# Optimization experiments

Measured on AMD Instinct MI355X. Metric: run time of the kernel, lower is better.

## Reference

```python
import jax, jax.numpy as jnp
import numpy as np

N_NODES = 100000
N_EDGES = 3200000
IN_DIM = 62
OUT_DIM = 16
EDGE_DIM = 2


def setup_inputs() -> dict:
    key = jax.random.key(0)
    ks = jax.random.split(key, 8)
    h = jax.random.normal(ks[0], (N_NODES, IN_DIM), dtype=jnp.float32)
    e = jax.random.normal(ks[1], (N_EDGES, EDGE_DIM), dtype=jnp.float32)
    src = jax.random.randint(ks[2], (N_EDGES,), 0, N_NODES, dtype=jnp.int32)
    dst = jax.random.randint(ks[3], (N_EDGES,), 0, N_NODES, dtype=jnp.int32)
    # xavier-normal-ish scaled weights
    W_fc = jax.random.normal(ks[4], (OUT_DIM, IN_DIM), dtype=jnp.float32) * 0.2
    W_attn = jax.random.normal(ks[5], (1, 2 * OUT_DIM + EDGE_DIM), dtype=jnp.float32) * 0.2
    W_edge = jax.random.normal(ks[6], (EDGE_DIM, EDGE_DIM), dtype=jnp.float32) * 0.5
    W_e2n = jax.random.normal(ks[7], (OUT_DIM, EDGE_DIM), dtype=jnp.float32) * 0.5
    return {"h": h, "e": e, "src": src, "dst": dst, "W_fc": W_fc,
            "W_attn": W_attn, "W_edge": W_edge, "W_e2n": W_e2n}


def _agat_forward(h, e, src, dst, W_fc, W_attn, W_edge, W_e2n):
    n = h.shape[0]
    d = W_fc.shape[0]
    z = h @ W_fc.T                      # [N, D]
    ex = e @ W_edge.T                   # [E, edge_dim]
    # attn_fc([z_src, z_dst, ex]) split into per-part projections
    Wa_src = W_attn[:, :d]              # [1, D]
    Wa_dst = W_attn[:, d:2 * d]         # [1, D]
    Wa_e = W_attn[:, 2 * d:]            # [1, edge_dim]
    a_src = (z @ Wa_src.T)[:, 0]        # [N] per-node, gathered per-edge
    a_dst = (z @ Wa_dst.T)[:, 0]        # [N]
    a = a_src[src] + a_dst[dst] + (ex @ Wa_e.T)[:, 0]   # [E]
    e_att = jax.nn.leaky_relu(a, negative_slope=0.01)    # [E]
    # segment softmax over incoming edges of each dst node
    m = jax.ops.segment_max(e_att, dst, num_segments=n)  # [N]
    w = jnp.exp(e_att - m[dst])                           # [E]
    denom = jax.ops.segment_sum(w, dst, num_segments=n)   # [N]
    attn = w / denom[dst]                                  # [E]
    # message = z_src + ez; aggregated as attn-weighted sum (matches
    # sum(attn*z) + sum(attn*ez) in reduce_func)
    ez = ex @ W_e2n.T                                      # [E, D]
    msg = attn[:, None] * (z[src] + ez)                    # [E, D]
    return jax.ops.segment_sum(msg, dst, num_segments=n)   # [N, D]


def reference(h, e, src, dst, W_fc, W_attn, W_edge, W_e2n):
    return _agat_forward(h, e, src, dst, W_fc, W_attn, W_edge, W_e2n)
```

## Files before the change

### kernel.cpp

```cpp
#include <hip/hip_runtime.h>
#include <hip/hip_fp16.h>
#include <hip/hip_cooperative_groups.h>

namespace cg = cooperative_groups;

#define N_NODES 100000
#define N_EDGES 3200000
#define IN_DIM  62
#define OUT_DIM 16

#define EBC    4096
#define EPT    4
#define NEB    ((N_EDGES + EBC - 1) / EBC)
#define NPB    ((N_NODES + 1023) / 1024)
#define NBUCK  ((N_NODES + 63) / 64)
#define CAPL   4096
#define CSTR   16
#define NCU    256

typedef int nat_i2 __attribute__((ext_vector_type(2)));

struct AppendSh {
    int  cnt[NBUCK];
    int  pfx[NBUCK];
    int  combo[NBUCK];
    int2 pay[EBC];
    unsigned short pbkt[EBC];
    int  wsum[16];
};
struct GatherSh {
    int2 rec[CAPL];
    unsigned short inv[CAPL];
    unsigned int exb[CAPL];
    int hist[64], pfx[64], cur[64];
    float adst_l[64];
};
union ShArena { AppendSh a; GatherSh g; };

__device__ __forceinline__ void do_proj(
    int u, int tid,
    const float* __restrict__ h, const float* __restrict__ W_fc,
    const float* __restrict__ W_attn,
    __half* __restrict__ zh, float* __restrict__ a_src_arr,
    float* __restrict__ a_dst_arr)
{
    int i = u * 1024 + tid;
    if (i >= N_NODES) return;

    float acc[OUT_DIM];
#pragma unroll
    for (int j = 0; j < OUT_DIM; ++j) acc[j] = 0.f;

    const float2* __restrict__ hr = (const float2*)(h + (size_t)i * IN_DIM);
#pragma unroll
    for (int kk = 0; kk < IN_DIM / 2; ++kk) {
        float2 hv = hr[kk];
#pragma unroll
        for (int j = 0; j < OUT_DIM; ++j) {
            acc[j] += hv.x * W_fc[j * IN_DIM + 2 * kk]
                    + hv.y * W_fc[j * IN_DIM + 2 * kk + 1];
        }
    }

    float asrc = 0.f, adst = 0.f;
#pragma unroll
    for (int j = 0; j < OUT_DIM; ++j) {
        asrc += acc[j] * W_attn[j];
        adst += acc[j] * W_attn[OUT_DIM + j];
    }

    union { __half hx[16]; uint4 q[2]; } uq;
#pragma unroll
    for (int j = 0; j < OUT_DIM; ++j) uq.hx[j] = __float2half(acc[j]);
    uint4* __restrict__ zrow = (uint4*)(zh + (size_t)i * OUT_DIM);
    zrow[0] = uq.q[0];
    zrow[1] = uq.q[1];

    a_src_arr[i] = asrc;
    a_dst_arr[i] = adst;
}

__device__ __forceinline__ void do_append(
    int be, int tid, AppendSh& S,
    const float* __restrict__ e, const int* __restrict__ src,
    const int* __restrict__ dst, int* __restrict__ cursor,
    nat_i2* __restrict__ records, int cap)
{
    __syncthreads();

    long ebase = (long)be * EBC;
    int chunk_n = (int)min((long)EBC, (long)N_EDGES - ebase);

    int dv[EPT], sv[EPT];
    float2 ev[EPT];
#pragma unroll
    for (int j = 0; j < EPT; ++j) {
        int p = tid + j * 1024;
        dv[j] = -1;
        if (p < chunk_n) {
            long eid = ebase + p;
            dv[j] = dst[eid];
            sv[j] = src[eid];
            ev[j] = ((const float2*)e)[eid];
        }
    }

    for (int t = tid; t < NBUCK; t += 1024) S.cnt[t] = 0;
    __syncthreads();

#pragma unroll
    for (int j = 0; j < EPT; ++j)
        if (dv[j] >= 0) atomicAdd(&S.cnt[dv[j] >> 6], 1);
    __syncthreads();

    int b0 = 2 * tid, b1 = b0 + 1;
    int c0 = (b0 < NBUCK) ? S.cnt[b0] : 0;
    int c1 = (b1 < NBUCK) ? S.cnt[b1] : 0;
    if (b0 < NBUCK) S.cnt[b0] = 0;
    if (b1 < NBUCK) S.cnt[b1] = 0;
    int gb0 = 0, gb1 = 0;
    if (c0) gb0 = atomicAdd(&cursor[b0 * CSTR], c0);
    if (c1) gb1 = atomicAdd(&cursor[b1 * CSTR], c1);

    int ts = c0 + c1;
    {
        int lane = tid & 63, wid = tid >> 6;
        int x = ts;
#pragma unroll
        for (int off = 1; off < 64; off <<= 1) {
            int y = __shfl_up(x, off, 64);
            if (lane >= off) x += y;
        }
        if (lane == 63) S.wsum[wid] = x;
        __syncthreads();
        if (wid == 0) {
            int v = (lane < 16) ? S.wsum[lane] : 0;
#pragma unroll
            for (int off = 1; off < 16; off <<= 1) {
                int y = __shfl_up(v, off, 64);
                if (lane >= off) v += y;
            }
            if (lane < 16) S.wsum[lane] = v;
        }
        __syncthreads();
        int texcl = x - ts + (wid ? S.wsum[wid - 1] : 0);
        if (b0 < NBUCK) { S.pfx[b0] = texcl;      S.combo[b0] = b0 * cap + gb0 - texcl; }
        if (b1 < NBUCK) { S.pfx[b1] = texcl + c0; S.combo[b1] = b1 * cap + gb1 - (texcl + c0); }
    }
    __syncthreads();

#pragma unroll
    for (int j = 0; j < EPT; ++j) {
        if (dv[j] >= 0) {
            int b = dv[j] >> 6;
            union { __half2 h2; int i; } uu;
            uu.h2.x = __float2half(ev[j].x);
            uu.h2.y = __float2half(ev[j].y);
            int r = atomicAdd(&S.cnt[b], 1);
            int q = S.pfx[b] + r;
            S.pay[q]  = make_int2(uu.i, sv[j] | ((dv[j] & 63) << 17));
            S.pbkt[q] = (unsigned short)b;
        }
    }
    __syncthreads();

    for (int p = tid; p < chunk_n; p += 1024) {
        int2 v  = S.pay[p];
        int  bb = S.pbkt[p];
        int pos = S.combo[bb] + p;
        if (pos < (bb + 1) * cap) {
            nat_i2 vv; vv.x = v.x; vv.y = v.y;
            __builtin_nontemporal_store(vv, records + pos);
        }
    }
}

__device__ __forceinline__ void do_gather(
    int b, int tid, GatherSh& S,
    const int* __restrict__ cursor, const nat_i2* __restrict__ records,
    const __half* __restrict__ zh, const float* __restrict__ a_src_arr,
    const float* __restrict__ a_dst_arr, const float* __restrict__ W_attn,
    const float* __restrict__ W_edge, const float* __restrict__ W_e2n,
    float* __restrict__ out, int cap)
{
    __syncthreads();

    long lo = (long)b * cap;
    int n   = cursor[b * CSTR];
    int nl  = n < cap ? n : cap;

    if (tid < 64) {
        S.hist[tid] = 0; S.cur[tid] = 0;
        int node = (b << 6) + tid;
        S.adst_l[tid] = (node < N_NODES) ? a_dst_arr[node] : 0.f;
    }
    __syncthreads();

    float we00 = W_edge[0], we01 = W_edge[1], we10 = W_edge[2], we11 = W_edge[3];
    float wa0  = W_attn[2 * OUT_DIM], wa1 = W_attn[2 * OUT_DIM + 1];

    int ld0 = -1, ld1 = -1, ld2 = -1, ld3 = -1;
#define EDGEW(J, LD)                                                        \
    {                                                                       \
        int k = tid + (J) * 1024;                                           \
        if (k < nl) {                                                       \
            nat_i2 r = __builtin_nontemporal_load(records + lo + k);        \
            int s  = r.y & 0x1FFFF;                                         \
            LD     = (r.y >> 17) & 63;                                      \
            union { int i; __half2 h2; } ue; ue.i = r.x;                    \
            float e0 = __low2float(ue.h2), e1 = __high2float(ue.h2);        \
            float ex0 = e0 * we00 + e1 * we01;                              \
            float ex1 = e0 * we10 + e1 * we11;                              \
            float a = a_src_arr[s] + S.adst_l[LD] + ex0 * wa0 + ex1 * wa1;  \
            float ea = (a > 0.f) ? a : 0.01f * a;                           \
            float w  = __expf(ea);                                          \
            S.rec[k] = make_int2(__float_as_int(w), r.y);                   \
            union { unsigned int i; __half2 h2; } up;                       \
            up.h2.x = __float2half(ex0);                                    \
            up.h2.y = __float2half(ex1);                                    \
            S.exb[k] = up.i;                                                \
            atomicAdd(&S.hist[LD], 1);                                      \
        }                                                                   \
    }
    EDGEW(0, ld0) EDGEW(1, ld1) EDGEW(2, ld2) EDGEW(3, ld3)
#undef EDGEW
    __syncthreads();

    if (tid < 64) S.pfx[tid] = S.hist[tid];
    __syncthreads();
    for (int off = 1; off < 64; off <<= 1) {
        int t = 0;
        if (tid < 64 && tid >= off) t = S.pfx[tid - off];
        __syncthreads();
        if (tid < 64) S.pfx[tid] += t;
        __syncthreads();
    }
    if (tid < 64) S.pfx[tid] -= S.hist[tid];
    __syncthreads();

#define INVW(J, LD)                                                         \
    if (LD >= 0) {                                                          \
        int k = tid + (J) * 1024;                                           \
        int r = atomicAdd(&S.cur[LD], 1);                                   \
        S.inv[S.pfx[LD] + r] = (unsigned short)k;                           \
    }
    INVW(0, ld0) INVW(1, ld1) INVW(2, ld2) INVW(3, ld3)
#undef INVW
    __syncthreads();

    int ld   = tid >> 4;
    int lane = tid & 15;
    int node = (b << 6) + ld;

    int m    = S.hist[ld];
    int base = S.pfx[ld];

    float acc0 = 0.f, acc1 = 0.f, accw0 = 0.f, accw1 = 0.f;
    float ax00 = 0.f, ax01 = 0.f, ax10 = 0.f, ax11 = 0.f;

    int i = 0;
    for (; i + 1 < m; i += 2) {
        int k0 = S.inv[base + i];
        int k1 = S.inv[base + i + 1];
        int2 r0 = S.rec[k0];
        int2 r1 = S.rec[k1];
        float w0 = __int_as_float(r0.x);
        float w1 = __int_as_float(r1.x);
        int s0 = r0.y & 0x1FFFF;
        int s1 = r1.y & 0x1FFFF;
        union { unsigned int i; __half2 h2; } x0, x1;
        x0.i = S.exb[k0];
        x1.i = S.exb[k1];

        float zv0 = __half2float(zh[s0 * OUT_DIM + lane]);
        float zv1 = __half2float(zh[s1 * OUT_DIM + lane]);

        acc0  += w0 * zv0;                 acc1  += w1 * zv1;
        accw0 += w0;                       accw1 += w1;
        ax00  += w0 * __low2float(x0.h2);  ax01  += w1 * __low2float(x1.h2);
        ax10  += w0 * __high2float(x0.h2); ax11  += w1 * __high2float(x1.h2);
    }
    if (i < m) {
        int k0 = S.inv[base + i];
        int2 r0 = S.rec[k0];
        float w0 = __int_as_float(r0.x);
        int s0 = r0.y & 0x1FFFF;
        union { unsigned int i; __half2 h2; } x0;
        x0.i = S.exb[k0];
        float zv0 = __half2float(zh[s0 * OUT_DIM + lane]);
        acc0  += w0 * zv0;
        accw0 += w0;
        ax00  += w0 * __low2float(x0.h2);
        ax10  += w0 * __high2float(x0.h2);
    }

    if (node < N_NODES) {
        float acc  = acc0 + acc1;
        float accw = accw0 + accw1;
        float ax0  = ax00 + ax01;
        float ax1  = ax10 + ax11;

        float ez   = ax0 * W_e2n[2 * lane] + ax1 * W_e2n[2 * lane + 1];
        float invw = (accw != 0.f) ? (1.f / accw) : 0.f;
        out[(size_t)node * OUT_DIM + lane] = (acc + ez) * invw;
    }
}

__global__ __launch_bounds__(1024) void fused_kernel(
    const float* __restrict__ h, const float* __restrict__ e,
    const int* __restrict__ src, const int* __restrict__ dst,
    const float* __restrict__ W_fc, const float* __restrict__ W_attn,
    const float* __restrict__ W_edge, const float* __restrict__ W_e2n,
    __half* __restrict__ zh, float* __restrict__ a_src_arr,
    float* __restrict__ a_dst_arr, int* __restrict__ cursor,
    nat_i2* __restrict__ records, float* __restrict__ out, int cap)
{
    __shared__ ShArena sh;
    cg::grid_group grid = cg::this_grid();
    int tid = threadIdx.x;

    for (int t = blockIdx.x * 1024 + tid; t < NBUCK * CSTR; t += gridDim.x * 1024)
        cursor[t] = 0;
    grid.sync();

    for (int u = blockIdx.x; u < NPB + NEB; u += gridDim.x) {
        if (u < NPB) do_proj(u, tid, h, W_fc, W_attn, zh, a_src_arr, a_dst_arr);
        else         do_append(u - NPB, tid, sh.a, e, src, dst, cursor, records, cap);
    }
    grid.sync();

    for (int b = blockIdx.x; b < NBUCK; b += gridDim.x)
        do_gather(b, tid, sh.g, cursor, records, zh, a_src_arr, a_dst_arr,
                  W_attn, W_edge, W_e2n, out, cap);
}

__global__ __launch_bounds__(1024) void proj_append_kernel(
    const float* __restrict__ h, const float* __restrict__ W_fc,
    const float* __restrict__ W_attn, const float* __restrict__ e,
    const int* __restrict__ src, const int* __restrict__ dst,
    __half* __restrict__ zh, float* __restrict__ a_src_arr,
    float* __restrict__ a_dst_arr, int* __restrict__ cursor,
    nat_i2* __restrict__ records, int cap)
{
    __shared__ AppendSh sh;
    if (blockIdx.x < NPB)
        do_proj(blockIdx.x, threadIdx.x, h, W_fc, W_attn, zh, a_src_arr, a_dst_arr);
    else
        do_append(blockIdx.x - NPB, threadIdx.x, sh, e, src, dst, cursor, records, cap);
}

__global__ __launch_bounds__(1024) void bucket_gather_kernel(
    const int* __restrict__ cursor, const nat_i2* __restrict__ records,
    const __half* __restrict__ zh, const float* __restrict__ a_src_arr,
    const float* __restrict__ a_dst_arr, const float* __restrict__ W_attn,
    const float* __restrict__ W_edge, const float* __restrict__ W_e2n,
    float* __restrict__ out, int cap)
{
    __shared__ GatherSh sh;
    do_gather(blockIdx.x, threadIdx.x, sh, cursor, records, zh,
              a_src_arr, a_dst_arr, W_attn, W_edge, W_e2n, out, cap);
}


__global__ __launch_bounds__(256) void node_proj_fb_kernel(
    const float* __restrict__ h,
    const float* __restrict__ W_fc,
    const float* __restrict__ W_attn,
    float* __restrict__ z,
    float* __restrict__ a_src_arr,
    float* __restrict__ a_dst_arr,
    float* __restrict__ denom,
    float* __restrict__ out)
{
    int i = blockIdx.x * blockDim.x + threadIdx.x;
    if (i >= N_NODES) return;

    float acc[OUT_DIM];
#pragma unroll
    for (int j = 0; j < OUT_DIM; ++j) acc[j] = 0.f;

    const float2* __restrict__ hr = (const float2*)(h + (size_t)i * IN_DIM);
#pragma unroll
    for (int kk = 0; kk < IN_DIM / 2; ++kk) {
        float2 hv = hr[kk];
#pragma unroll
        for (int j = 0; j < OUT_DIM; ++j) {
            acc[j] += hv.x * W_fc[j * IN_DIM + 2 * kk]
                    + hv.y * W_fc[j * IN_DIM + 2 * kk + 1];
        }
    }

    float asrc = 0.f, adst = 0.f;
#pragma unroll
    for (int j = 0; j < OUT_DIM; ++j) {
        asrc += acc[j] * W_attn[j];
        adst += acc[j] * W_attn[OUT_DIM + j];
    }

    float4* __restrict__ zrow = (float4*)(z + (size_t)i * OUT_DIM);
    zrow[0] = make_float4(acc[0],  acc[1],  acc[2],  acc[3]);
    zrow[1] = make_float4(acc[4],  acc[5],  acc[6],  acc[7]);
    zrow[2] = make_float4(acc[8],  acc[9],  acc[10], acc[11]);
    zrow[3] = make_float4(acc[12], acc[13], acc[14], acc[15]);

    a_src_arr[i] = asrc;
    a_dst_arr[i] = adst;
    denom[i] = 0.f;

    float4 z4 = make_float4(0.f, 0.f, 0.f, 0.f);
    float4* __restrict__ orow = (float4*)(out + (size_t)i * OUT_DIM);
    orow[0] = z4; orow[1] = z4; orow[2] = z4; orow[3] = z4;
}

__global__ __launch_bounds__(256) void edge_kernel(
    const float* __restrict__ e,
    const int*   __restrict__ src,
    const int*   __restrict__ dst,
    const float* __restrict__ W_attn,
    const float* __restrict__ W_edge,
    const float* __restrict__ W_e2n,
    const float* __restrict__ z,
    const float* __restrict__ a_src_arr,
    const float* __restrict__ a_dst_arr,
    float* __restrict__ denom,
    float* __restrict__ out)
{
    int eid = blockIdx.x * blockDim.x + threadIdx.x;
    if (eid >= N_EDGES) return;

    int s = src[eid];
    int d = dst[eid];

    float2 ev = ((const float2*)e)[eid];
    float ex0 = ev.x * W_edge[0] + ev.y * W_edge[1];
    float ex1 = ev.x * W_edge[2] + ev.y * W_edge[3];

    float a = a_src_arr[s] + a_dst_arr[d]
            + ex0 * W_attn[2 * OUT_DIM] + ex1 * W_attn[2 * OUT_DIM + 1];
    float ea = (a > 0.f) ? a : 0.01f * a;
    float w  = __expf(ea);

    unsafeAtomicAdd(denom + d, w);

    const float4* __restrict__ zrow = (const float4*)(z + (size_t)s * OUT_DIM);
    float4 z0 = zrow[0], z1 = zrow[1], z2 = zrow[2], z3 = zrow[3];

    float* __restrict__ orow = out + (size_t)d * OUT_DIM;
    float zs[OUT_DIM] = { z0.x, z0.y, z0.z, z0.w,
                          z1.x, z1.y, z1.z, z1.w,
                          z2.x, z2.y, z2.z, z2.w,
                          z3.x, z3.y, z3.z, z3.w };
#pragma unroll
    for (int j = 0; j < OUT_DIM; ++j) {
        float ez = ex0 * W_e2n[2 * j] + ex1 * W_e2n[2 * j + 1];
        unsafeAtomicAdd(orow + j, w * (zs[j] + ez));
    }
}

__global__ __launch_bounds__(256) void normalize_kernel(
    float* __restrict__ out, const float* __restrict__ denom)
{
    int tid = blockIdx.x * blockDim.x + threadIdx.x;
    const int total = N_NODES * OUT_DIM / 4;
    if (tid >= total) return;
    int n = tid >> 2;
    float dn = denom[n];
    float inv = (dn != 0.f) ? (1.f / dn) : 0.f;
    float4 v = ((float4*)out)[tid];
    v.x *= inv; v.y *= inv; v.z *= inv; v.w *= inv;
    ((float4*)out)[tid] = v;
}

extern "C" void kernel_launch(void* const* d_in, const int* in_sizes, int n_in,
                              void* d_out, int out_size, void* d_ws, size_t ws_size,
                              hipStream_t stream)
{
    const float* h      = (const float*)d_in[0];
    const float* e      = (const float*)d_in[1];
    const int*   src    = (const int*)  d_in[2];
    const int*   dst    = (const int*)  d_in[3];
    const float* W_fc   = (const float*)d_in[4];
    const float* W_attn = (const float*)d_in[5];
    const float* W_edge = (const float*)d_in[6];
    const float* W_e2n  = (const float*)d_in[7];
    float* out = (float*)d_out;

    char* ws = (char*)d_ws;

    size_t off = 0;
    __half* zh        = (__half*)(ws + off); off += (size_t)N_NODES * OUT_DIM * 2;
    float*  a_src_arr = (float*) (ws + off); off += (size_t)N_NODES * 4;
    float*  a_dst_arr = (float*) (ws + off); off += (size_t)N_NODES * 4;
    off = (off + 255) & ~(size_t)255;
    int*    cursor = (int*)(ws + off);
    size_t  cur_bytes = (size_t)NBUCK * CSTR * 4;
    off += (cur_bytes + 255) & ~(size_t)255;
    size_t rec_off = (off + 255) & ~(size_t)255;

    int cap = 0;
    if      (ws_size >= rec_off + (size_t)NBUCK * 4096 * 8) cap = 4096;
    else if (ws_size >= rec_off + (size_t)NBUCK * 3072 * 8) cap = 3072;
    else if (ws_size >= rec_off + (size_t)NBUCK * 2560 * 8) cap = 2560;
    else if (ws_size >= rec_off + (size_t)NBUCK * 2304 * 8) cap = 2304;

    if (cap) {
        nat_i2* records = (nat_i2*)(ws + rec_off);

        hipError_t lerr = hipErrorUnknown;
        int maxB = 0;
        hipError_t qerr = hipOccupancyMaxActiveBlocksPerMultiprocessor(
            &maxB, reinterpret_cast<const void*>(fused_kernel), 1024, 0);
        if (qerr == hipSuccess && maxB > 0) {
            int gridB = (maxB >= 2 ? 2 : 1) * NCU;
            void* kargs[] = {
                (void*)&h, (void*)&e, (void*)&src, (void*)&dst,
                (void*)&W_fc, (void*)&W_attn, (void*)&W_edge, (void*)&W_e2n,
                (void*)&zh, (void*)&a_src_arr, (void*)&a_dst_arr,
                (void*)&cursor, (void*)&records, (void*)&out, (void*)&cap };
            lerr = hipLaunchCooperativeKernel(
                reinterpret_cast<const void*>(fused_kernel),
                dim3(gridB), dim3(1024), kargs, 0, stream);
        }

        if (lerr != hipSuccess) {
            hipMemsetAsync(cursor, 0, cur_bytes, stream);

            proj_append_kernel<<<NPB + NEB, 1024, 0, stream>>>(
                h, W_fc, W_attn, e, src, dst,
                zh, a_src_arr, a_dst_arr, cursor, records, cap);

            bucket_gather_kernel<<<NBUCK, 1024, 0, stream>>>(
                cursor, records, zh, a_src_arr, a_dst_arr,
                W_attn, W_edge, W_e2n, out, cap);
        }
    } else {
        size_t foff = 0;
        float* z     = (float*)(ws + foff); foff += (size_t)N_NODES * OUT_DIM * 4;
        float* asrc  = (float*)(ws + foff); foff += (size_t)N_NODES * 4;
        float* adst  = (float*)(ws + foff); foff += (size_t)N_NODES * 4;
        float* denom = (float*)(ws + foff); foff += (size_t)N_NODES * 4;

        node_proj_fb_kernel<<<(N_NODES + 255) / 256, 256, 0, stream>>>(
            h, W_fc, W_attn, z, asrc, adst, denom, out);

        edge_kernel<<<(N_EDGES + 255) / 256, 256, 0, stream>>>(
            e, src, dst, W_attn, W_edge, W_e2n, z, asrc, adst, denom, out);

        normalize_kernel<<<(N_NODES * OUT_DIM / 4 + 255) / 256, 256, 0, stream>>>(
            out, denom);
    }
}
```

Measured before the change: 240.0 us.

## Replace global atomic bucket cursors with count-scan-append deterministic placement

Replaces the global atomicAdd cursor reservation per bucket with a three-phase scheme. Each edge chunk first counts its edges per bucket into a counts matrix. A per-bucket warp scan then computes base offsets and totals, and a second append pass writes records at the precomputed positions. This removes contention on global atomics and the cursor memset, but dst is read twice, a counts/bases matrix of NEB×NBUCK is added (about 1.2M ints each), and the cooperative kernel gains two more grid syncs.

```diff
diff --git a/kernel.cpp b/kernel.cpp
--- a/kernel.cpp
+++ b/kernel.cpp
@@ -15,7 +15,6 @@
 #define NPB    ((N_NODES + 1023) / 1024)
 #define NBUCK  ((N_NODES + 63) / 64)
 #define CAPL   4096
-#define CSTR   16
 #define NCU    256
 
 typedef int nat_i2 __attribute__((ext_vector_type(2)));
@@ -80,10 +79,49 @@
     a_dst_arr[i] = adst;
 }
 
+__device__ __forceinline__ void do_count(
+    int be, int tid, AppendSh& S,
+    const int* __restrict__ dst, int* __restrict__ counts)
+{
+    __syncthreads();
+    for (int t = tid; t < NBUCK; t += 1024) S.cnt[t] = 0;
+    __syncthreads();
+
+    long ebase = (long)be * EBC;
+    int chunk_n = (int)min((long)EBC, (long)N_EDGES - ebase);
+    for (int p = tid; p < chunk_n; p += 1024)
+        atomicAdd(&S.cnt[dst[ebase + p] >> 6], 1);
+    __syncthreads();
+
+    int* col = counts + (size_t)be * NBUCK;
+    for (int t = tid; t < NBUCK; t += 1024) col[t] = S.cnt[t];
+}
+
+__device__ __forceinline__ void do_scan_bucket(
+    int b, int lane, const int* __restrict__ counts,
+    int* __restrict__ bases, int* __restrict__ totals)
+{
+    int run = 0;
+#pragma unroll
+    for (int k = 0; k < (NEB + 63) / 64; ++k) {
+        int be = k * 64 + lane;
+        int c = (be < NEB) ? counts[(size_t)be * NBUCK + b] : 0;
+        int x = c;
+#pragma unroll
+        for (int off = 1; off < 64; off <<= 1) {
+            int y = __shfl_up(x, off, 64);
+            if (lane >= off) x += y;
+        }
+        if (be < NEB) bases[(size_t)b * NEB + be] = run + x - c;
+        run += __shfl(x, 63, 64);
+    }
+    if (lane == 0) totals[b] = run;
+}
+
 __device__ __forceinline__ void do_append(
     int be, int tid, AppendSh& S,
     const float* __restrict__ e, const int* __restrict__ src,
-    const int* __restrict__ dst, int* __restrict__ cursor,
+    const int* __restrict__ dst, const int* __restrict__ bases,
     nat_i2* __restrict__ records, int cap)
 {
     __syncthreads();
@@ -119,8 +157,8 @@
     if (b0 < NBUCK) S.cnt[b0] = 0;
     if (b1 < NBUCK) S.cnt[b1] = 0;
     int gb0 = 0, gb1 = 0;
-    if (c0) gb0 = atomicAdd(&cursor[b0 * CSTR], c0);
-    if (c1) gb1 = atomicAdd(&cursor[b1 * CSTR], c1);
+    if (b0 < NBUCK) gb0 = bases[(size_t)b0 * NEB + be];
+    if (b1 < NBUCK) gb1 = bases[(size_t)b1 * NEB + be];
 
     int ts = c0 + c1;
     {
@@ -177,7 +215,7 @@
 
 __device__ __forceinline__ void do_gather(
     int b, int tid, GatherSh& S,
-    const int* __restrict__ cursor, const nat_i2* __restrict__ records,
+    const int* __restrict__ totals, const nat_i2* __restrict__ records,
     const __half* __restrict__ zh, const float* __restrict__ a_src_arr,
     const float* __restrict__ a_dst_arr, const float* __restrict__ W_attn,
     const float* __restrict__ W_edge, const float* __restrict__ W_e2n,
@@ -186,7 +224,7 @@
     __syncthreads();
 
     long lo = (long)b * cap;
-    int n   = cursor[b * CSTR];
+    int n   = totals[b];
     int nl  = n < cap ? n : cap;
 
     if (tid < 64) {
@@ -312,52 +350,77 @@
     const float* __restrict__ W_fc, const float* __restrict__ W_attn,
     const float* __restrict__ W_edge, const float* __restrict__ W_e2n,
     __half* __restrict__ zh, float* __restrict__ a_src_arr,
-    float* __restrict__ a_dst_arr, int* __restrict__ cursor,
+    float* __restrict__ a_dst_arr, int* __restrict__ counts,
+    int* __restrict__ bases, int* __restrict__ totals,
     nat_i2* __restrict__ records, float* __restrict__ out, int cap)
 {
     __shared__ ShArena sh;
     cg::grid_group grid = cg::this_grid();
     int tid = threadIdx.x;
 
-    for (int t = blockIdx.x * 1024 + tid; t < NBUCK * CSTR; t += gridDim.x * 1024)
-        cursor[t] = 0;
-    grid.sync();
-
     for (int u = blockIdx.x; u < NPB + NEB; u += gridDim.x) {
         if (u < NPB) do_proj(u, tid, h, W_fc, W_attn, zh, a_src_arr, a_dst_arr);
-        else         do_append(u - NPB, tid, sh.a, e, src, dst, cursor, records, cap);
+        else         do_count(u - NPB, tid, sh.a, dst, counts);
     }
     grid.sync();
 
+    {
+        int lane = tid & 63;
+        int gw   = blockIdx.x * (1024 / 64) + (tid >> 6);
+        for (int b = gw; b < NBUCK; b += gridDim.x * (1024 / 64))
+            do_scan_bucket(b, lane, counts, bases, totals);
+    }
+    grid.sync();
+
+    for (int u = blockIdx.x; u < NEB; u += gridDim.x)
+        do_append(u, tid, sh.a, e, src, dst, bases, records, cap);
+    grid.sync();
+
     for (int b = blockIdx.x; b < NBUCK; b += gridDim.x)
-        do_gather(b, tid, sh.g, cursor, records, zh, a_src_arr, a_dst_arr,
+        do_gather(b, tid, sh.g, totals, records, zh, a_src_arr, a_dst_arr,
                   W_attn, W_edge, W_e2n, out, cap);
 }
 
-__global__ __launch_bounds__(1024) void proj_append_kernel(
+__global__ __launch_bounds__(1024) void proj_count_kernel(
     const float* __restrict__ h, const float* __restrict__ W_fc,
-    const float* __restrict__ W_attn, const float* __restrict__ e,
-    const int* __restrict__ src, const int* __restrict__ dst,
+    const float* __restrict__ W_attn, const int* __restrict__ dst,
     __half* __restrict__ zh, float* __restrict__ a_src_arr,
-    float* __restrict__ a_dst_arr, int* __restrict__ cursor,
-    nat_i2* __restrict__ records, int cap)
+    float* __restrict__ a_dst_arr, int* __restrict__ counts)
 {
     __shared__ AppendSh sh;
     if (blockIdx.x < NPB)
         do_proj(blockIdx.x, threadIdx.x, h, W_fc, W_attn, zh, a_src_arr, a_dst_arr);
     else
-        do_append(blockIdx.x - NPB, threadIdx.x, sh, e, src, dst, cursor, records, cap);
-}
-
-__global__ __launch_bounds__(1024) void bucket_gather_kernel(
-    const int* __restrict__ cursor, const nat_i2* __restrict__ records,
+        do_count(blockIdx.x - NPB, threadIdx.x, sh, dst, counts);
+}
+
+__global__ __launch_bounds__(256) void scan_kernel(
+    const int* __restrict__ counts, int* __restrict__ bases,
+    int* __restrict__ totals)
+{
+    int lane = threadIdx.x & 63;
+    int gw   = blockIdx.x * 4 + (threadIdx.x >> 6);
+    if (gw < NBUCK) do_scan_bucket(gw, lane, counts, bases, totals);
+}
+
+__global__ __launch_bounds__(1024) void append_kernel(
+    const float* __restrict__ e, const int* __restrict__ src,
+    const int* __restrict__ dst, const int* __restrict__ bases,
+    nat_i2* __restrict__ records, int cap)
+{
+    __shared__ AppendSh sh;
+    do_append(blockIdx.x, threadIdx.x, sh, e, src, dst, bases, records, cap);
+}
+
+__global__ __launch_bounds__(1024) void gather_kernel(
+    const int* __restrict__ totals, const nat_i2* __restrict__ records,
     const __half* __restrict__ zh, const float* __restrict__ a_src_arr,
     const float* __restrict__ a_dst_arr, const float* __restrict__ W_attn,
     const float* __restrict__ W_edge, const float* __restrict__ W_e2n,
     float* __restrict__ out, int cap)
 {
     __shared__ GatherSh sh;
-    do_gather(blockIdx.x, threadIdx.x, sh, cursor, records, zh,
+    do_gather(blockIdx.x, threadIdx.x, sh, totals, records, zh,
               a_src_arr, a_dst_arr, W_attn, W_edge, W_e2n, out, cap);
 }
 
@@ -492,9 +555,9 @@
     float*  a_src_arr = (float*) (ws + off); off += (size_t)N_NODES * 4;
     float*  a_dst_arr = (float*) (ws + off); off += (size_t)N_NODES * 4;
     off = (off + 255) & ~(size_t)255;
-    int*    cursor = (int*)(ws + off);
-    size_t  cur_bytes = (size_t)NBUCK * CSTR * 4;
-    off += (cur_bytes + 255) & ~(size_t)255;
+    int* totals = (int*)(ws + off); off += ((size_t)NBUCK * 4 + 255) & ~(size_t)255;
+    int* counts = (int*)(ws + off); off += ((size_t)NEB * NBUCK * 4 + 255) & ~(size_t)255;
+    int* bases  = (int*)(ws + off); off += ((size_t)NBUCK * NEB * 4 + 255) & ~(size_t)255;
     size_t rec_off = (off + 255) & ~(size_t)255;
 
     int cap = 0;
@@ -516,21 +579,25 @@
                 (void*)&h, (void*)&e, (void*)&src, (void*)&dst,
                 (void*)&W_fc, (void*)&W_attn, (void*)&W_edge, (void*)&W_e2n,
                 (void*)&zh, (void*)&a_src_arr, (void*)&a_dst_arr,
-                (void*)&cursor, (void*)&records, (void*)&out, (void*)&cap };
+                (void*)&counts, (void*)&bases, (void*)&totals,
+                (void*)&records, (void*)&out, (void*)&cap };
             lerr = hipLaunchCooperativeKernel(
                 reinterpret_cast<const void*>(fused_kernel),
                 dim3(gridB), dim3(1024), kargs, 0, stream);
         }
 
         if (lerr != hipSuccess) {
-            hipMemsetAsync(cursor, 0, cur_bytes, stream);
-
-            proj_append_kernel<<<NPB + NEB, 1024, 0, stream>>>(
-                h, W_fc, W_attn, e, src, dst,
-                zh, a_src_arr, a_dst_arr, cursor, records, cap);
-
-            bucket_gather_kernel<<<NBUCK, 1024, 0, stream>>>(
-                cursor, records, zh, a_src_arr, a_dst_arr,
+            proj_count_kernel<<<NPB + NEB, 1024, 0, stream>>>(
+                h, W_fc, W_attn, dst, zh, a_src_arr, a_dst_arr, counts);
+
+            scan_kernel<<<(NBUCK + 3) / 4, 256, 0, stream>>>(
+                counts, bases, totals);
+
+            append_kernel<<<NEB, 1024, 0, stream>>>(
+                e, src, dst, bases, records, cap);
+
+            gather_kernel<<<NBUCK, 1024, 0, stream>>>(
+                totals, records, zh, a_src_arr, a_dst_arr,
                 W_attn, W_edge, W_e2n, out, cap);
         }
     } else {
```

Result: slower. 251.2 us (+4.7%).
